# Optimization experiments

Hardware: AMD Instinct MI355X
Metric: run time of the kernel (lower is better)

## Reference

```python
import jax, jax.numpy as jnp
import numpy as np

D_MODEL = 1024
N_HEADS = 16
D_K = D_MODEL // N_HEADS


def setup_inputs() -> dict:
    key = jax.random.key(0)
    ks = jax.random.split(key, 11)
    B, S = 2, 2048
    scale = 1.0 / np.sqrt(D_MODEL)
    inp = {
        "q": jax.random.normal(ks[0], (B, S, D_MODEL), jnp.float32),
        "k": jax.random.normal(ks[1], (B, S, D_MODEL), jnp.float32),
        "v": jax.random.normal(ks[2], (B, S, D_MODEL), jnp.float32),
        "w_q": jax.random.normal(ks[3], (D_MODEL, D_MODEL), jnp.float32) * scale,
        "b_q": jnp.zeros((D_MODEL,), jnp.float32),
        "w_k": jax.random.normal(ks[4], (D_MODEL, D_MODEL), jnp.float32) * scale,
        "b_k": jnp.zeros((D_MODEL,), jnp.float32),
        "w_v": jax.random.normal(ks[5], (D_MODEL, D_MODEL), jnp.float32) * scale,
        "b_v": jnp.zeros((D_MODEL,), jnp.float32),
        "w_o": jax.random.normal(ks[6], (D_MODEL, D_MODEL), jnp.float32) * scale,
        "b_o": jnp.zeros((D_MODEL,), jnp.float32),
    }
    return inp


def reference(q, k, v, w_q, b_q, w_k, b_k, w_v, b_v, w_o, b_o):
    B, S, _ = q.shape
    # Linear projections (torch Linear: x @ W.T + b), split heads -> [B, H, S, d_k]
    def proj(x, w, b):
        y = x @ w.T + b
        return y.reshape(B, -1, N_HEADS, D_K).transpose(0, 2, 1, 3)

    qh = proj(q, w_q, b_q)
    kh = proj(k, w_k, b_k)
    vh = proj(v, w_v, b_v)

    scores = jnp.einsum("bhsd,bhtd->bhst", qh, kh) / np.sqrt(D_K)  # [B,H,S,S]
    attn = jax.nn.softmax(scores, axis=-1)  # dropout is identity at eval
    out = jnp.einsum("bhst,bhtd->bhsd", attn, vh)  # [B,H,S,d_k]
    out = out.transpose(0, 2, 1, 3).reshape(B, S, N_HEADS * D_K)
    return out @ w_o.T + b_o
```

## Files before the change

kernel.cpp:

```cpp
#include <hip/hip_runtime.h>
#include <cstdint>


typedef float  f32x4   __attribute__((ext_vector_type(4)));
typedef float  f32x16  __attribute__((ext_vector_type(16)));
typedef __bf16 bf16x8  __attribute__((ext_vector_type(8)));
typedef unsigned short u16;
typedef u16 u16x4 __attribute__((ext_vector_type(4)));
typedef u16 u16x8 __attribute__((ext_vector_type(8)));

#define D_MODEL 1024
#define SEQ     2048
#define BATCH   2
#define NH      16
#define DKH     64
#define MTOT    (BATCH * SEQ)
#define KVB     64
#define QBLK    256
#define HSTRIDE ((size_t)SEQ * DKH)

#if __has_builtin(__builtin_amdgcn_exp2f)
#define EXP2(x) __builtin_amdgcn_exp2f(x)
#else
#define EXP2(x) exp2f(x)
#endif

__device__ __forceinline__ u16 f2bf(float f) {
  uint32_t u = __builtin_bit_cast(uint32_t, f);
  u = u + 0x7fffu + ((u >> 16) & 1u);
  return (u16)(u >> 16);
}
__device__ __forceinline__ u16 f2bf_hw(float f) {
  return __builtin_bit_cast(u16, (__bf16)f);
}

__device__ __forceinline__ void gl_lds16(const void* g, void* l) {
  __builtin_amdgcn_global_load_lds(
      (__attribute__((address_space(1))) void*)(g),
      (__attribute__((address_space(3))) void*)(l), 16, 0, 0);
}

__device__ __forceinline__ void cvt_body(const float* __restrict__ in,
                                         u16* __restrict__ out, int i) {
  float4 v = reinterpret_cast<const float4*>(in)[i];
  uint32_t p0 = (uint32_t)f2bf(v.x) | ((uint32_t)f2bf(v.y) << 16);
  uint32_t p1 = (uint32_t)f2bf(v.z) | ((uint32_t)f2bf(v.w) << 16);
  reinterpret_cast<uint2*>(out)[i] = make_uint2(p0, p1);
}

__global__ __launch_bounds__(256) void cvt_qkv(
    const float* q, const float* k, const float* v,
    u16* qb, u16* kb, u16* vb) {
  int z = blockIdx.y;
  const float* in = (z == 0) ? q : (z == 1) ? k : v;
  u16* out = (z == 0) ? qb : (z == 1) ? kb : vb;
  cvt_body(in, out, blockIdx.x * 256 + threadIdx.x);
}

__global__ __launch_bounds__(256) void cvt_w(
    const float* w0, const float* w1, const float* w2, const float* w3,
    u16* o0, u16* o1, u16* o2, u16* o3) {
  int z = blockIdx.y;
  const float* in = (z == 0) ? w0 : (z == 1) ? w1 : (z == 2) ? w2 : w3;
  u16* out = (z == 0) ? o0 : (z == 1) ? o1 : (z == 2) ? o2 : o3;
  cvt_body(in, out, blockIdx.x * 256 + threadIdx.x);
}

template <bool BF16OUT, bool HEADA, bool HEADC>
__device__ __forceinline__ void gemm_bt_body(
    const u16* __restrict__ A, const u16* __restrict__ W,
    const float* __restrict__ bias, void* __restrict__ Cout,
    int N, int K, float scale, int bidx) {
  __shared__ u16 As[128][64];
  __shared__ u16 Bs[128][64];
  const int nbx = N / 128;
  const int bx = bidx % nbx, by = bidx / nbx;
  const int tid = threadIdx.x, wave = tid >> 6, lane = tid & 63;
  const int l15 = lane & 15, lg = lane >> 4;
  const int wr = wave >> 1, wc = wave & 1;
  f32x4 acc[4][4] = {};
  const int rA = by * 128 + (lane >> 3);
  const int rB = bx * 128 + (lane >> 3);
  const int ccol = (lane & 7) * 8;

  for (int kt = 0; kt < K; kt += 64) {
    for (int c = wave; c < 16; c += 4) {
      if (HEADA) {
        int m = rA + 8 * c;
        size_t a_off = (size_t)((m >> 11) * NH + (kt >> 6)) * HSTRIDE +
                       (size_t)(m & (SEQ - 1)) * 64 + ccol;
        gl_lds16(A + a_off, &As[8 * c][0]);
      } else {
        gl_lds16(A + (size_t)(rA + 8 * c) * K + kt + ccol, &As[8 * c][0]);
      }
      gl_lds16(W + (size_t)(rB + 8 * c) * K + kt + ccol, &Bs[8 * c][0]);
    }
    __syncthreads();
#pragma unroll
    for (int kc = 0; kc < 2; ++kc) {
      bf16x8 af[4], bw[4];
#pragma unroll
      for (int m = 0; m < 4; ++m)
        af[m] = *(const bf16x8*)&As[wr * 64 + m * 16 + l15][kc * 32 + 8 * lg];
#pragma unroll
      for (int n = 0; n < 4; ++n)
        bw[n] = *(const bf16x8*)&Bs[wc * 64 + n * 16 + l15][kc * 32 + 8 * lg];
#pragma unroll
      for (int m = 0; m < 4; ++m)
#pragma unroll
        for (int n = 0; n < 4; ++n)
          acc[m][n] = __builtin_amdgcn_mfma_f32_16x16x32_bf16(
              af[m], bw[n], acc[m][n], 0, 0, 0);
    }
    __syncthreads();
  }
#pragma unroll
  for (int n = 0; n < 4; ++n) {
    int col = bx * 128 + wc * 64 + n * 16 + l15;
    float bv = bias[col];
#pragma unroll
    for (int m = 0; m < 4; ++m) {
      int row0 = by * 128 + wr * 64 + m * 16 + 4 * lg;
#pragma unroll
      for (int j = 0; j < 4; ++j) {
        float v = (acc[m][n][j] + bv) * scale;
        int row = row0 + j;
        if (HEADC) {
          size_t off = (size_t)((row >> 11) * NH + (col >> 6)) * HSTRIDE +
                       (size_t)(row & (SEQ - 1)) * 64 + (col & 63);
          ((u16*)Cout)[off] = f2bf(v);
        } else if (BF16OUT) {
          ((u16*)Cout)[(size_t)row * N + col] = f2bf(v);
        } else {
          ((float*)Cout)[(size_t)row * N + col] = v;
        }
      }
    }
  }
}

#define SCALE_Q 0.18033688011112042f

__global__ __launch_bounds__(256) void proj_kernel(
    const u16* qb, const u16* kb, const u16* vb,
    const u16* wq, const u16* wk, const u16* wv,
    const float* b_q, const float* b_k, const float* b_v,
    u16* Qp, u16* Kp, u16* Vp) {
  int z = blockIdx.y;
  const u16* A = (z == 0) ? qb : (z == 1) ? kb : vb;
  const u16* W = (z == 0) ? wq : (z == 1) ? wk : wv;
  const float* bi = (z == 0) ? b_q : (z == 1) ? b_k : b_v;
  u16* O = (z == 0) ? Qp : (z == 1) ? Kp : Vp;
  float scale = (z == 0) ? SCALE_Q : 1.0f;
  gemm_bt_body<true, false, true>(A, W, bi, O, D_MODEL, D_MODEL, scale,
                                  blockIdx.x);
}

__global__ __launch_bounds__(256) void oproj_kernel(
    const u16* Op, const u16* wo, const float* b_o, float* out) {
  gemm_bt_body<false, true, false>(Op, wo, b_o, out, D_MODEL, D_MODEL, 1.0f,
                                   blockIdx.x);
}

__global__ __launch_bounds__(512, 2) void attn_kernel(
    const u16* __restrict__ Qh, const u16* __restrict__ Kh,
    const u16* __restrict__ Vh, u16* __restrict__ Oh) {
  __shared__ u16 QPl[QBLK * 64];
  __shared__ u16 Ks[2][KVB * 64];
  __shared__ u16 Vt[2][64 * KVB];
  const int bid = blockIdx.x;
  const int g = bid & 31, qt = bid >> 5;
  const size_t base = (size_t)g * HSTRIDE;
  const int tid = threadIdx.x, wave = tid >> 6, lane = tid & 63;
  const int l31 = lane & 31, hi = lane >> 5;
  const int q0 = qt * QBLK;
  const int srow = lane >> 3;
  const int scol = 8 * ((lane & 7) ^ srow);

  for (int c = wave; c < 32; c += 8)
    gl_lds16(Qh + base + (size_t)(q0 + 8 * c + srow) * 64 + scol,
             QPl + 8 * c * 64);
  gl_lds16(Kh + base + (size_t)(8 * wave + srow) * 64 + scol,
           Ks[0] + 8 * wave * 64);
  const int vp = tid >> 4, vq = tid & 15;
  u16x4 va, vb;
  {
    const u16* vsrc = Vh + base + (size_t)(2 * vp) * 64 + vq * 4;
    va = *(const u16x4*)vsrc;
    vb = *(const u16x4*)(vsrc + 64);
  }
  asm volatile("s_waitcnt vmcnt(0)" ::: "memory");
  __syncthreads();
#pragma unroll
  for (int j = 0; j < 4; ++j) {
    int dk = vq * 4 + j;
    uint32_t wv = (uint32_t)va[j] | ((uint32_t)vb[j] << 16);
    *(uint32_t*)&Vt[0][dk * 64 + (((vp >> 2) ^ (vq & 7)) << 3) + (vp & 3) * 2] =
        wv;
  }
  __syncthreads();

  bf16x8 qf[4];
#pragma unroll
  for (int kk = 0; kk < 4; ++kk) {
    int row = wave * 32 + l31;
    qf[kk] = *(const bf16x8*)&QPl[row * 64 + (((2 * kk + hi) ^ (row & 7)) << 3)];
  }
  u16* Pw = QPl + wave * 32 * 64;

  float mrow = -3e38f, lrow = 0.f;
  f32x16 acc[2] = {};

  for (int kt = 0; kt < SEQ / KVB; ++kt) {
    const int cur = kt & 1, nxt = cur ^ 1;
    if (kt + 1 < SEQ / KVB) {
      const size_t kv0 = base + (size_t)(kt + 1) * KVB * 64;
      gl_lds16(Kh + kv0 + (size_t)(8 * wave + srow) * 64 + scol,
               Ks[nxt] + 8 * wave * 64);
      const u16* vsrc = Vh + kv0 + (size_t)(2 * vp) * 64 + vq * 4;
      va = *(const u16x4*)vsrc;
      vb = *(const u16x4*)(vsrc + 64);
    }
    f32x16 s[2] = {};
#pragma unroll
    for (int t = 0; t < 2; ++t)
#pragma unroll
      for (int kk = 0; kk < 4; ++kk) {
        int row = t * 32 + l31;
        bf16x8 kf = *(const bf16x8*)&Ks[cur][row * 64 +
                                             (((2 * kk + hi) ^ (row & 7)) << 3)];
        s[t] = __builtin_amdgcn_mfma_f32_32x32x16_bf16(kf, qf[kk], s[t], 0, 0, 0);
      }
    float mx[16];
#pragma unroll
    for (int r = 0; r < 16; ++r) mx[r] = fmaxf(s[0][r], s[1][r]);
#pragma unroll
    for (int st2 = 8; st2 >= 1; st2 >>= 1)
#pragma unroll
      for (int r = 0; r < st2; ++r) mx[r] = fmaxf(mx[r], mx[r + st2]);
    float mtile = fmaxf(mx[0], __shfl_xor(mx[0], 32, 64));
    float mnew = fmaxf(mrow, mtile);
    float corr = EXP2(mrow - mnew);
    mrow = mnew;
    float sm0 = 0.f, sm1 = 0.f, sm2 = 0.f, sm3 = 0.f;
#pragma unroll
    for (int t = 0; t < 2; ++t)
#pragma unroll
      for (int r = 0; r < 16; r += 4) {
        float p0 = EXP2(s[t][r] - mnew);
        float p1 = EXP2(s[t][r + 1] - mnew);
        float p2 = EXP2(s[t][r + 2] - mnew);
        float p3 = EXP2(s[t][r + 3] - mnew);
        s[t][r] = p0; s[t][r + 1] = p1; s[t][r + 2] = p2; s[t][r + 3] = p3;
        sm0 += p0; sm1 += p1; sm2 += p2; sm3 += p3;
      }
    float psum = (sm0 + sm1) + (sm2 + sm3);
    lrow = lrow * corr + (psum + __shfl_xor(psum, 32, 64));
#pragma unroll
    for (int nd = 0; nd < 2; ++nd)
#pragma unroll
      for (int r = 0; r < 16; ++r) acc[nd][r] *= corr;

#pragma unroll
    for (int t = 0; t < 2; ++t)
#pragma unroll
      for (int b2 = 0; b2 < 4; ++b2) {
        u16x4 pk = {f2bf_hw(s[t][4 * b2]), f2bf_hw(s[t][4 * b2 + 1]),
                    f2bf_hw(s[t][4 * b2 + 2]), f2bf_hw(s[t][4 * b2 + 3])};
        *(u16x4*)&Pw[l31 * 64 + (((4 * t + b2) ^ (l31 & 7)) << 3) + 4 * hi] = pk;
      }
#pragma unroll
    for (int ks = 0; ks < 4; ++ks) {
      bf16x8 pf =
          *(const bf16x8*)&Pw[l31 * 64 + (((2 * ks + hi) ^ (l31 & 7)) << 3)];
#pragma unroll
      for (int nd = 0; nd < 2; ++nd) {
        int dkr = nd * 32 + l31;
        bf16x8 vf = *(const bf16x8*)&Vt[cur][dkr * 64 +
                        (((2 * ks + hi) ^ ((l31 >> 2) & 7)) << 3)];
        acc[nd] =
            __builtin_amdgcn_mfma_f32_32x32x16_bf16(vf, pf, acc[nd], 0, 0, 0);
      }
    }
    asm volatile("s_waitcnt vmcnt(0)" ::: "memory");
    __syncthreads();
    if (kt + 1 < SEQ / KVB) {
#pragma unroll
      for (int j = 0; j < 4; ++j) {
        int dk = vq * 4 + j;
        uint32_t wv = (uint32_t)va[j] | ((uint32_t)vb[j] << 16);
        *(uint32_t*)&Vt[nxt][dk * 64 + (((vp >> 2) ^ (vq & 7)) << 3) +
                             (vp & 3) * 2] = wv;
      }
    }
    __syncthreads();
  }

  float rinv = 1.0f / lrow;
  u16* Os = QPl;
  {
    int row = wave * 32 + l31;
#pragma unroll
    for (int nd = 0; nd < 2; ++nd)
#pragma unroll
      for (int b2 = 0; b2 < 4; ++b2) {
        u16x4 ok = {f2bf_hw(acc[nd][4 * b2] * rinv),
                    f2bf_hw(acc[nd][4 * b2 + 1] * rinv),
                    f2bf_hw(acc[nd][4 * b2 + 2] * rinv),
                    f2bf_hw(acc[nd][4 * b2 + 3] * rinv)};
        *(u16x4*)&Os[row * 64 + (((4 * nd + b2) ^ (row & 7)) << 3) + 4 * hi] =
            ok;
      }
  }
  __syncthreads();
  {
    const int row = tid >> 1, half = tid & 1;
    u16* gp = (u16*)(Oh + base + (size_t)(q0 + row) * 64 + half * 32);
#pragma unroll
    for (int c2 = 0; c2 < 4; ++c2) {
      int pc = (half * 4 + c2) ^ (row & 7);
      *(u16x8*)(gp + c2 * 8) = *(const u16x8*)&Os[row * 64 + pc * 8];
    }
  }
}

extern "C" void kernel_launch(void* const* d_in, const int* in_sizes, int n_in,
                              void* d_out, int out_size, void* d_ws,
                              size_t ws_size, hipStream_t stream) {
  (void)in_sizes; (void)n_in; (void)out_size; (void)ws_size;
  const float* q   = (const float*)d_in[0];
  const float* k   = (const float*)d_in[1];
  const float* v   = (const float*)d_in[2];
  const float* w_q = (const float*)d_in[3];
  const float* b_q = (const float*)d_in[4];
  const float* w_k = (const float*)d_in[5];
  const float* b_k = (const float*)d_in[6];
  const float* w_v = (const float*)d_in[7];
  const float* b_v = (const float*)d_in[8];
  const float* w_o = (const float*)d_in[9];
  const float* b_o = (const float*)d_in[10];
  float* out = (float*)d_out;

  const size_t ACT = (size_t)MTOT * D_MODEL;
  const size_t WEL = (size_t)D_MODEL * D_MODEL;
  u16* qb  = (u16*)d_ws;
  u16* kb  = qb + ACT;
  u16* vb  = kb + ACT;
  u16* wqb = vb + ACT;
  u16* wkb = wqb + WEL;
  u16* wvb = wkb + WEL;
  u16* wob = wvb + WEL;
  u16* Qp  = wob + WEL;
  u16* Kp  = Qp + ACT;
  u16* Vp  = Kp + ACT;
  u16* Op  = Vp + ACT;

  const int na = (int)(ACT / 4), nw = (int)(WEL / 4);
  cvt_qkv<<<dim3(na / 256, 3), 256, 0, stream>>>(q, k, v, qb, kb, vb);
  cvt_w<<<dim3(nw / 256, 4), 256, 0, stream>>>(w_q, w_k, w_v, w_o,
                                               wqb, wkb, wvb, wob);

  proj_kernel<<<dim3((MTOT / 128) * (D_MODEL / 128), 3), 256, 0, stream>>>(
      qb, kb, vb, wqb, wkb, wvb, b_q, b_k, b_v, Qp, Kp, Vp);

  attn_kernel<<<dim3(BATCH * NH * (SEQ / QBLK)), 512, 0, stream>>>(Qp, Kp, Vp,
                                                                   Op);

  oproj_kernel<<<dim3((MTOT / 128) * (D_MODEL / 128)), 256, 0, stream>>>(
      Op, wob, b_o, out);
}
```

Before: 249.0 us.

## Split KV range across wave halves, lazy rescale, merge conversion kernels

The attention kernel now uses a 128-row Q block. Its 8 waves split into two halves that each cover half of the KV sequence, and their partial softmax states are merged through LDS at the end. This doubles the grid and raises occupancy (launch bounds 4). It also adds lazy max rescaling that skips the correction unless the tile max grows by more than 8, sets MFMA priority hints, and replaces the async K prefetch with register-staged loads. The two fp32-to-bf16 conversion launches are merged into one. The costs are an extra merge step and more sync per tile, and the lazy rescale lets exponentials reach up to 2^8, which is a precision risk.

Result: slower. 293.0 us (+17.7%).

```diff
diff --git a/kernel.cpp b/kernel.cpp
--- a/kernel.cpp
+++ b/kernel.cpp
@@ -16,7 +16,7 @@
 #define DKH     64
 #define MTOT    (BATCH * SEQ)
 #define KVB     64
-#define QBLK    256
+#define QBLK    128
 #define HSTRIDE ((size_t)SEQ * DKH)
 
 #if __has_builtin(__builtin_amdgcn_exp2f)
@@ -48,22 +48,23 @@
   reinterpret_cast<uint2*>(out)[i] = make_uint2(p0, p1);
 }
 
-__global__ __launch_bounds__(256) void cvt_qkv(
+__global__ __launch_bounds__(256) void cvt_all(
     const float* q, const float* k, const float* v,
-    u16* qb, u16* kb, u16* vb) {
-  int z = blockIdx.y;
-  const float* in = (z == 0) ? q : (z == 1) ? k : v;
-  u16* out = (z == 0) ? qb : (z == 1) ? kb : vb;
-  cvt_body(in, out, blockIdx.x * 256 + threadIdx.x);
-}
-
-__global__ __launch_bounds__(256) void cvt_w(
     const float* w0, const float* w1, const float* w2, const float* w3,
-    u16* o0, u16* o1, u16* o2, u16* o3) {
-  int z = blockIdx.y;
-  const float* in = (z == 0) ? w0 : (z == 1) ? w1 : (z == 2) ? w2 : w3;
-  u16* out = (z == 0) ? o0 : (z == 1) ? o1 : (z == 2) ? o2 : o3;
-  cvt_body(in, out, blockIdx.x * 256 + threadIdx.x);
+    u16* qb, u16* kb, u16* vb, u16* o0, u16* o1, u16* o2, u16* o3) {
+  const int NA = 1 << 20, NW = 1 << 18;
+  int i = blockIdx.x * 256 + threadIdx.x;
+  const float* src; u16* dst; int r;
+  if (i < 3 * NA) {
+    int s = i >> 20; r = i & (NA - 1);
+    src = (s == 0) ? q : (s == 1) ? k : v;
+    dst = (s == 0) ? qb : (s == 1) ? kb : vb;
+  } else {
+    int j = i - 3 * NA; int s = j >> 18; r = j & (NW - 1);
+    src = (s == 0) ? w0 : (s == 1) ? w1 : (s == 2) ? w2 : w3;
+    dst = (s == 0) ? o0 : (s == 1) ? o1 : (s == 2) ? o2 : o3;
+  }
+  cvt_body(src, dst, r);
 }
 
 template <bool BF16OUT, bool HEADA, bool HEADC>
@@ -162,75 +163,90 @@
                                    blockIdx.x);
 }
 
-__global__ __launch_bounds__(512, 2) void attn_kernel(
+__global__ __launch_bounds__(512, 4) void attn_kernel(
     const u16* __restrict__ Qh, const u16* __restrict__ Kh,
     const u16* __restrict__ Vh, u16* __restrict__ Oh) {
-  __shared__ u16 QPl[QBLK * 64];
-  __shared__ u16 Ks[2][KVB * 64];
-  __shared__ u16 Vt[2][64 * KVB];
+  __shared__ u16 QPl[16384];
+  __shared__ u16 Ks[2][4096];
+  __shared__ u16 Vt[2][4096];
   const int bid = blockIdx.x;
   const int g = bid & 31, qt = bid >> 5;
   const size_t base = (size_t)g * HSTRIDE;
   const int tid = threadIdx.x, wave = tid >> 6, lane = tid & 63;
   const int l31 = lane & 31, hi = lane >> 5;
+  const int qg = wave & 3, half = wave >> 2;
   const int q0 = qt * QBLK;
   const int srow = lane >> 3;
   const int scol = 8 * ((lane & 7) ^ srow);
 
-  for (int c = wave; c < 32; c += 8)
+  const int ht = tid & 255;
+  const int kr = ht >> 2, kc4 = ht & 3;
+  const int vp2 = ht >> 3, vd8 = (ht & 7) * 8;
+  const size_t kvbase = base + (size_t)(half * (SEQ / 2)) * 64;
+
+  for (int c = wave; c < 16; c += 8)
     gl_lds16(Qh + base + (size_t)(q0 + 8 * c + srow) * 64 + scol,
              QPl + 8 * c * 64);
-  gl_lds16(Kh + base + (size_t)(8 * wave + srow) * 64 + scol,
-           Ks[0] + 8 * wave * 64);
-  const int vp = tid >> 4, vq = tid & 15;
-  u16x4 va, vb;
+  u16x8 kra, krb, va, vb;
   {
-    const u16* vsrc = Vh + base + (size_t)(2 * vp) * 64 + vq * 4;
-    va = *(const u16x4*)vsrc;
-    vb = *(const u16x4*)(vsrc + 64);
+    const u16* ks = Kh + kvbase + (size_t)kr * 64 + kc4 * 16;
+    kra = *(const u16x8*)ks;
+    krb = *(const u16x8*)(ks + 8);
+    const u16* vs = Vh + kvbase + (size_t)(2 * vp2) * 64 + vd8;
+    va = *(const u16x8*)vs;
+    vb = *(const u16x8*)(vs + 64);
   }
   asm volatile("s_waitcnt vmcnt(0)" ::: "memory");
   __syncthreads();
-#pragma unroll
-  for (int j = 0; j < 4; ++j) {
-    int dk = vq * 4 + j;
-    uint32_t wv = (uint32_t)va[j] | ((uint32_t)vb[j] << 16);
-    *(uint32_t*)&Vt[0][dk * 64 + (((vp >> 2) ^ (vq & 7)) << 3) + (vp & 3) * 2] =
-        wv;
-  }
+#define STORE_KV()                                                         \
+  {                                                                        \
+    *(u16x8*)&Ks[half][kr * 64 + (((2 * kc4) ^ (kr & 7)) << 3)] = kra;     \
+    *(u16x8*)&Ks[half][kr * 64 + (((2 * kc4 + 1) ^ (kr & 7)) << 3)] = krb; \
+    _Pragma("unroll") for (int d = 0; d < 8; ++d) {                        \
+      int dk = vd8 + d;                                                    \
+      uint32_t wv = (uint32_t)va[d] | ((uint32_t)vb[d] << 16);             \
+      *(uint32_t*)&Vt[half][dk * 64 + (((vp2 >> 2) ^ ((dk >> 2) & 7)) << 3) + \
+                            (vp2 & 3) * 2] = wv;                           \
+    }                                                                      \
+  }
+  STORE_KV();
   __syncthreads();
 
   bf16x8 qf[4];
 #pragma unroll
   for (int kk = 0; kk < 4; ++kk) {
-    int row = wave * 32 + l31;
+    int row = qg * 32 + l31;
     qf[kk] = *(const bf16x8*)&QPl[row * 64 + (((2 * kk + hi) ^ (row & 7)) << 3)];
   }
-  u16* Pw = QPl + wave * 32 * 64;
+  __syncthreads();
+  u16* Pw = QPl + wave * 2048;
 
   float mrow = -3e38f, lrow = 0.f;
   f32x16 acc[2] = {};
-
-  for (int kt = 0; kt < SEQ / KVB; ++kt) {
-    const int cur = kt & 1, nxt = cur ^ 1;
-    if (kt + 1 < SEQ / KVB) {
-      const size_t kv0 = base + (size_t)(kt + 1) * KVB * 64;
-      gl_lds16(Kh + kv0 + (size_t)(8 * wave + srow) * 64 + scol,
-               Ks[nxt] + 8 * wave * 64);
-      const u16* vsrc = Vh + kv0 + (size_t)(2 * vp) * 64 + vq * 4;
-      va = *(const u16x4*)vsrc;
-      vb = *(const u16x4*)(vsrc + 64);
+  const int NT = (SEQ / 2) / KVB;
+
+  for (int kt = 0; kt < NT; ++kt) {
+    if (kt + 1 < NT) {
+      const size_t kvo = kvbase + (size_t)(kt + 1) * KVB * 64;
+      const u16* ks = Kh + kvo + (size_t)kr * 64 + kc4 * 16;
+      kra = *(const u16x8*)ks;
+      krb = *(const u16x8*)(ks + 8);
+      const u16* vs = Vh + kvo + (size_t)(2 * vp2) * 64 + vd8;
+      va = *(const u16x8*)vs;
+      vb = *(const u16x8*)(vs + 64);
     }
     f32x16 s[2] = {};
+    __builtin_amdgcn_s_setprio(1);
 #pragma unroll
     for (int t = 0; t < 2; ++t)
 #pragma unroll
       for (int kk = 0; kk < 4; ++kk) {
         int row = t * 32 + l31;
-        bf16x8 kf = *(const bf16x8*)&Ks[cur][row * 64 +
-                                             (((2 * kk + hi) ^ (row & 7)) << 3)];
+        bf16x8 kf = *(const bf16x8*)&Ks[half][row * 64 +
+                                              (((2 * kk + hi) ^ (row & 7)) << 3)];
         s[t] = __builtin_amdgcn_mfma_f32_32x32x16_bf16(kf, qf[kk], s[t], 0, 0, 0);
       }
+    __builtin_amdgcn_s_setprio(0);
     float mx[16];
 #pragma unroll
     for (int r = 0; r < 16; ++r) mx[r] = fmaxf(s[0][r], s[1][r]);
@@ -239,27 +255,29 @@
 #pragma unroll
       for (int r = 0; r < st2; ++r) mx[r] = fmaxf(mx[r], mx[r + st2]);
     float mtile = fmaxf(mx[0], __shfl_xor(mx[0], 32, 64));
-    float mnew = fmaxf(mrow, mtile);
-    float corr = EXP2(mrow - mnew);
-    mrow = mnew;
+    if (mtile > mrow + 8.0f) {
+      float corr = EXP2(mrow - mtile);
+      mrow = mtile;
+      lrow *= corr;
+#pragma unroll
+      for (int nd = 0; nd < 2; ++nd)
+#pragma unroll
+        for (int r = 0; r < 16; ++r) acc[nd][r] *= corr;
+    }
     float sm0 = 0.f, sm1 = 0.f, sm2 = 0.f, sm3 = 0.f;
 #pragma unroll
     for (int t = 0; t < 2; ++t)
 #pragma unroll
       for (int r = 0; r < 16; r += 4) {
-        float p0 = EXP2(s[t][r] - mnew);
-        float p1 = EXP2(s[t][r + 1] - mnew);
-        float p2 = EXP2(s[t][r + 2] - mnew);
-        float p3 = EXP2(s[t][r + 3] - mnew);
+        float p0 = EXP2(s[t][r] - mrow);
+        float p1 = EXP2(s[t][r + 1] - mrow);
+        float p2 = EXP2(s[t][r + 2] - mrow);
+        float p3 = EXP2(s[t][r + 3] - mrow);
         s[t][r] = p0; s[t][r + 1] = p1; s[t][r + 2] = p2; s[t][r + 3] = p3;
         sm0 += p0; sm1 += p1; sm2 += p2; sm3 += p3;
       }
     float psum = (sm0 + sm1) + (sm2 + sm3);
-    lrow = lrow * corr + (psum + __shfl_xor(psum, 32, 64));
-#pragma unroll
-    for (int nd = 0; nd < 2; ++nd)
-#pragma unroll
-      for (int r = 0; r < 16; ++r) acc[nd][r] *= corr;
+    lrow += psum + __shfl_xor(psum, 32, 64);
 
 #pragma unroll
     for (int t = 0; t < 2; ++t)
@@ -269,36 +287,57 @@
                     f2bf_hw(s[t][4 * b2 + 2]), f2bf_hw(s[t][4 * b2 + 3])};
         *(u16x4*)&Pw[l31 * 64 + (((4 * t + b2) ^ (l31 & 7)) << 3) + 4 * hi] = pk;
       }
-#pragma unroll
-    for (int ks = 0; ks < 4; ++ks) {
+    __builtin_amdgcn_s_setprio(1);
+#pragma unroll
+    for (int ks2 = 0; ks2 < 4; ++ks2) {
       bf16x8 pf =
-          *(const bf16x8*)&Pw[l31 * 64 + (((2 * ks + hi) ^ (l31 & 7)) << 3)];
+          *(const bf16x8*)&Pw[l31 * 64 + (((2 * ks2 + hi) ^ (l31 & 7)) << 3)];
 #pragma unroll
       for (int nd = 0; nd < 2; ++nd) {
         int dkr = nd * 32 + l31;
-        bf16x8 vf = *(const bf16x8*)&Vt[cur][dkr * 64 +
-                        (((2 * ks + hi) ^ ((l31 >> 2) & 7)) << 3)];
+        bf16x8 vf = *(const bf16x8*)&Vt[half][dkr * 64 +
+                        (((2 * ks2 + hi) ^ ((l31 >> 2) & 7)) << 3)];
         acc[nd] =
             __builtin_amdgcn_mfma_f32_32x32x16_bf16(vf, pf, acc[nd], 0, 0, 0);
       }
     }
-    asm volatile("s_waitcnt vmcnt(0)" ::: "memory");
+    __builtin_amdgcn_s_setprio(0);
     __syncthreads();
-    if (kt + 1 < SEQ / KVB) {
-#pragma unroll
-      for (int j = 0; j < 4; ++j) {
-        int dk = vq * 4 + j;
-        uint32_t wv = (uint32_t)va[j] | ((uint32_t)vb[j] << 16);
-        *(uint32_t*)&Vt[nxt][dk * 64 + (((vp >> 2) ^ (vq & 7)) << 3) +
-                             (vp & 3) * 2] = wv;
-      }
-    }
+    if (kt + 1 < NT) STORE_KV();
     __syncthreads();
   }
 
-  float rinv = 1.0f / lrow;
-  u16* Os = QPl;
-  {
+  float* MA = (float*)QPl;
+  float* ML = (float*)Vt;
+  if (wave >= 4) {
+    int u = wave - 4;
+#pragma unroll
+    for (int j = 0; j < 8; ++j) {
+      f32x4 qd = {acc[j >> 2][4 * (j & 3)], acc[j >> 2][4 * (j & 3) + 1],
+                  acc[j >> 2][4 * (j & 3) + 2], acc[j >> 2][4 * (j & 3) + 3]};
+      *(f32x4*)&MA[u * 2048 + lane * 32 + ((j ^ (lane & 7)) << 2)] = qd;
+    }
+    ML[u * 128 + lane * 2] = mrow;
+    ML[u * 128 + lane * 2 + 1] = lrow;
+  }
+  __syncthreads();
+  u16* Os = &Ks[0][0];
+  if (wave < 4) {
+    float mb = ML[wave * 128 + lane * 2];
+    float lb = ML[wave * 128 + lane * 2 + 1];
+    float m2 = fmaxf(mrow, mb);
+    float ca = EXP2(mrow - m2), cb = EXP2(mb - m2);
+    lrow = lrow * ca + lb * cb;
+#pragma unroll
+    for (int j = 0; j < 8; ++j) {
+      f32x4 qd = *(const f32x4*)&MA[wave * 2048 + lane * 32 +
+                                    ((j ^ (lane & 7)) << 2)];
+#pragma unroll
+      for (int m = 0; m < 4; ++m)
+        acc[j >> 2][4 * (j & 3) + m] =
+            acc[j >> 2][4 * (j & 3) + m] * ca + qd[m] * cb;
+    }
+    float rinv = 1.0f / lrow;
     int row = wave * 32 + l31;
 #pragma unroll
     for (int nd = 0; nd < 2; ++nd)
@@ -314,12 +353,13 @@
   }
   __syncthreads();
   {
-    const int row = tid >> 1, half = tid & 1;
-    u16* gp = (u16*)(Oh + base + (size_t)(q0 + row) * 64 + half * 32);
-#pragma unroll
-    for (int c2 = 0; c2 < 4; ++c2) {
-      int pc = (half * 4 + c2) ^ (row & 7);
-      *(u16x8*)(gp + c2 * 8) = *(const u16x8*)&Os[row * 64 + pc * 8];
+    const int row = tid >> 2, cq = tid & 3;
+    u16* gp = (u16*)(Oh + base + (size_t)(q0 + row) * 64);
+#pragma unroll
+    for (int e = 0; e < 2; ++e) {
+      int c = 2 * cq + e;
+      *(u16x8*)(gp + c * 8) =
+          *(const u16x8*)&Os[row * 64 + ((c ^ (row & 7)) << 3)];
     }
   }
 }
@@ -355,10 +395,9 @@
   u16* Vp  = Kp + ACT;
   u16* Op  = Vp + ACT;
 
-  const int na = (int)(ACT / 4), nw = (int)(WEL / 4);
-  cvt_qkv<<<dim3(na / 256, 3), 256, 0, stream>>>(q, k, v, qb, kb, vb);
-  cvt_w<<<dim3(nw / 256, 4), 256, 0, stream>>>(w_q, w_k, w_v, w_o,
-                                               wqb, wkb, wvb, wob);
+  const int nq = (int)((3 * ACT + 4 * WEL) / 4);
+  cvt_all<<<nq / 256, 256, 0, stream>>>(q, k, v, w_q, w_k, w_v, w_o,
+                                        qb, kb, vb, wqb, wkb, wvb, wob);
 
   proj_kernel<<<dim3((MTOT / 128) * (D_MODEL / 128), 3), 256, 0, stream>>>(
       qb, kb, vb, wqb, wkb, wvb, b_q, b_k, b_v, Qp, Kp, Vp);
```

## Double KV tile per iteration, lazy softmax rescale, setprio, merged convert kernel

Applied to the files above, without the earlier changes.

The attention loop now handles 128 keys per iteration as two 64-key sub-tiles, which halves the number of barriers and loop iterations, with K/V LDS buffers grown to match. The online-softmax rescale of the accumulator and row sum is skipped unless some row's max has grown by more than 8 in log2 units. MFMA sections are wrapped in s_setprio to favour matrix issue. The two fp32-to-bf16 conversion kernels are merged into one launch. The costs are more LDS per block, which may reduce occupancy at 2 blocks per CU, and a softmax whose exponentials can reach up to 2^8 before rescaling.

New measurement: 243.9 us. -2.1%, faster.

```diff
diff --git a/kernel.cpp b/kernel.cpp
--- a/kernel.cpp
+++ b/kernel.cpp
@@ -15,7 +15,6 @@
 #define NH      16
 #define DKH     64
 #define MTOT    (BATCH * SEQ)
-#define KVB     64
 #define QBLK    256
 #define HSTRIDE ((size_t)SEQ * DKH)
 
@@ -48,22 +47,23 @@
   reinterpret_cast<uint2*>(out)[i] = make_uint2(p0, p1);
 }
 
-__global__ __launch_bounds__(256) void cvt_qkv(
+__global__ __launch_bounds__(256) void cvt_all(
     const float* q, const float* k, const float* v,
-    u16* qb, u16* kb, u16* vb) {
-  int z = blockIdx.y;
-  const float* in = (z == 0) ? q : (z == 1) ? k : v;
-  u16* out = (z == 0) ? qb : (z == 1) ? kb : vb;
-  cvt_body(in, out, blockIdx.x * 256 + threadIdx.x);
-}
-
-__global__ __launch_bounds__(256) void cvt_w(
     const float* w0, const float* w1, const float* w2, const float* w3,
-    u16* o0, u16* o1, u16* o2, u16* o3) {
-  int z = blockIdx.y;
-  const float* in = (z == 0) ? w0 : (z == 1) ? w1 : (z == 2) ? w2 : w3;
-  u16* out = (z == 0) ? o0 : (z == 1) ? o1 : (z == 2) ? o2 : o3;
-  cvt_body(in, out, blockIdx.x * 256 + threadIdx.x);
+    u16* qb, u16* kb, u16* vb, u16* o0, u16* o1, u16* o2, u16* o3) {
+  const int NA = 1 << 20, NW = 1 << 18;
+  int i = blockIdx.x * 256 + threadIdx.x;
+  const float* src; u16* dst; int r;
+  if (i < 3 * NA) {
+    int s = i >> 20; r = i & (NA - 1);
+    src = (s == 0) ? q : (s == 1) ? k : v;
+    dst = (s == 0) ? qb : (s == 1) ? kb : vb;
+  } else {
+    int j = i - 3 * NA; int s = j >> 18; r = j & (NW - 1);
+    src = (s == 0) ? w0 : (s == 1) ? w1 : (s == 2) ? w2 : w3;
+    dst = (s == 0) ? o0 : (s == 1) ? o1 : (s == 2) ? o2 : o3;
+  }
+  cvt_body(src, dst, r);
 }
 
 template <bool BF16OUT, bool HEADA, bool HEADC>
@@ -166,8 +166,8 @@
     const u16* __restrict__ Qh, const u16* __restrict__ Kh,
     const u16* __restrict__ Vh, u16* __restrict__ Oh) {
   __shared__ u16 QPl[QBLK * 64];
-  __shared__ u16 Ks[2][KVB * 64];
-  __shared__ u16 Vt[2][64 * KVB];
+  __shared__ u16 Ks[2][2][64 * 64];
+  __shared__ u16 Vt[2][2][64 * 64];
   const int bid = blockIdx.x;
   const int g = bid & 31, qt = bid >> 5;
   const size_t base = (size_t)g * HSTRIDE;
@@ -181,23 +181,31 @@
     gl_lds16(Qh + base + (size_t)(q0 + 8 * c + srow) * 64 + scol,
              QPl + 8 * c * 64);
   gl_lds16(Kh + base + (size_t)(8 * wave + srow) * 64 + scol,
-           Ks[0] + 8 * wave * 64);
+           &Ks[0][0][8 * wave * 64]);
+  gl_lds16(Kh + base + 4096 + (size_t)(8 * wave + srow) * 64 + scol,
+           &Ks[0][1][8 * wave * 64]);
   const int vp = tid >> 4, vq = tid & 15;
-  u16x4 va, vb;
+  u16x4 va, vb, vc, vd;
   {
-    const u16* vsrc = Vh + base + (size_t)(2 * vp) * 64 + vq * 4;
-    va = *(const u16x4*)vsrc;
-    vb = *(const u16x4*)(vsrc + 64);
+    const u16* vs = Vh + base + (size_t)(2 * vp) * 64 + vq * 4;
+    va = *(const u16x4*)vs;
+    vb = *(const u16x4*)(vs + 64);
+    vc = *(const u16x4*)(vs + 4096);
+    vd = *(const u16x4*)(vs + 4096 + 64);
   }
   asm volatile("s_waitcnt vmcnt(0)" ::: "memory");
   __syncthreads();
-#pragma unroll
-  for (int j = 0; j < 4; ++j) {
-    int dk = vq * 4 + j;
-    uint32_t wv = (uint32_t)va[j] | ((uint32_t)vb[j] << 16);
-    *(uint32_t*)&Vt[0][dk * 64 + (((vp >> 2) ^ (vq & 7)) << 3) + (vp & 3) * 2] =
-        wv;
-  }
+#define STORE_V(BUF, SUB, RA, RB)                                             \
+  {                                                                           \
+    _Pragma("unroll") for (int j = 0; j < 4; ++j) {                           \
+      int dk = vq * 4 + j;                                                    \
+      uint32_t wv = (uint32_t)RA[j] | ((uint32_t)RB[j] << 16);                \
+      *(uint32_t*)&Vt[BUF][SUB][dk * 64 + (((vp >> 2) ^ (vq & 7)) << 3) +     \
+                               (vp & 3) * 2] = wv;                            \
+    }                                                                         \
+  }
+  STORE_V(0, 0, va, vb);
+  STORE_V(0, 1, vc, vd);
   __syncthreads();
 
   bf16x8 qf[4];
@@ -210,88 +218,105 @@
 
   float mrow = -3e38f, lrow = 0.f;
   f32x16 acc[2] = {};
-
-  for (int kt = 0; kt < SEQ / KVB; ++kt) {
+  const int NT = SEQ / 128;
+
+  for (int kt = 0; kt < NT; ++kt) {
     const int cur = kt & 1, nxt = cur ^ 1;
-    if (kt + 1 < SEQ / KVB) {
-      const size_t kv0 = base + (size_t)(kt + 1) * KVB * 64;
+    if (kt + 1 < NT) {
+      const size_t kv0 = base + (size_t)(kt + 1) * 128 * 64;
       gl_lds16(Kh + kv0 + (size_t)(8 * wave + srow) * 64 + scol,
-               Ks[nxt] + 8 * wave * 64);
-      const u16* vsrc = Vh + kv0 + (size_t)(2 * vp) * 64 + vq * 4;
-      va = *(const u16x4*)vsrc;
-      vb = *(const u16x4*)(vsrc + 64);
-    }
-    f32x16 s[2] = {};
+               &Ks[nxt][0][8 * wave * 64]);
+      gl_lds16(Kh + kv0 + 4096 + (size_t)(8 * wave + srow) * 64 + scol,
+               &Ks[nxt][1][8 * wave * 64]);
+      const u16* vs = Vh + kv0 + (size_t)(2 * vp) * 64 + vq * 4;
+      va = *(const u16x4*)vs;
+      vb = *(const u16x4*)(vs + 64);
+      vc = *(const u16x4*)(vs + 4096);
+      vd = *(const u16x4*)(vs + 4096 + 64);
+    }
+    f32x16 s0[2] = {}, s1[2] = {};
+    __builtin_amdgcn_s_setprio(1);
 #pragma unroll
     for (int t = 0; t < 2; ++t)
 #pragma unroll
       for (int kk = 0; kk < 4; ++kk) {
         int row = t * 32 + l31;
-        bf16x8 kf = *(const bf16x8*)&Ks[cur][row * 64 +
-                                             (((2 * kk + hi) ^ (row & 7)) << 3)];
-        s[t] = __builtin_amdgcn_mfma_f32_32x32x16_bf16(kf, qf[kk], s[t], 0, 0, 0);
-      }
+        int off = row * 64 + (((2 * kk + hi) ^ (row & 7)) << 3);
+        s0[t] = __builtin_amdgcn_mfma_f32_32x32x16_bf16(
+            *(const bf16x8*)&Ks[cur][0][off], qf[kk], s0[t], 0, 0, 0);
+        s1[t] = __builtin_amdgcn_mfma_f32_32x32x16_bf16(
+            *(const bf16x8*)&Ks[cur][1][off], qf[kk], s1[t], 0, 0, 0);
+      }
+    __builtin_amdgcn_s_setprio(0);
     float mx[16];
 #pragma unroll
-    for (int r = 0; r < 16; ++r) mx[r] = fmaxf(s[0][r], s[1][r]);
+    for (int r = 0; r < 16; ++r)
+      mx[r] = fmaxf(fmaxf(s0[0][r], s0[1][r]), fmaxf(s1[0][r], s1[1][r]));
 #pragma unroll
     for (int st2 = 8; st2 >= 1; st2 >>= 1)
 #pragma unroll
       for (int r = 0; r < st2; ++r) mx[r] = fmaxf(mx[r], mx[r + st2]);
     float mtile = fmaxf(mx[0], __shfl_xor(mx[0], 32, 64));
-    float mnew = fmaxf(mrow, mtile);
-    float corr = EXP2(mrow - mnew);
-    mrow = mnew;
-    float sm0 = 0.f, sm1 = 0.f, sm2 = 0.f, sm3 = 0.f;
+    if (!__all(mtile - mrow <= 8.0f)) {
+      float mnew = fmaxf(mrow, mtile);
+      float corr = EXP2(mrow - mnew);
+      mrow = mnew;
+      lrow *= corr;
+#pragma unroll
+      for (int nd = 0; nd < 2; ++nd)
+#pragma unroll
+        for (int r = 0; r < 16; ++r) acc[nd][r] *= corr;
+    }
+    float sma = 0.f, smb = 0.f, smc = 0.f, smd = 0.f;
 #pragma unroll
     for (int t = 0; t < 2; ++t)
 #pragma unroll
       for (int r = 0; r < 16; r += 4) {
-        float p0 = EXP2(s[t][r] - mnew);
-        float p1 = EXP2(s[t][r + 1] - mnew);
-        float p2 = EXP2(s[t][r + 2] - mnew);
-        float p3 = EXP2(s[t][r + 3] - mnew);
-        s[t][r] = p0; s[t][r + 1] = p1; s[t][r + 2] = p2; s[t][r + 3] = p3;
-        sm0 += p0; sm1 += p1; sm2 += p2; sm3 += p3;
-      }
-    float psum = (sm0 + sm1) + (sm2 + sm3);
-    lrow = lrow * corr + (psum + __shfl_xor(psum, 32, 64));
-#pragma unroll
-    for (int nd = 0; nd < 2; ++nd)
-#pragma unroll
-      for (int r = 0; r < 16; ++r) acc[nd][r] *= corr;
-
-#pragma unroll
-    for (int t = 0; t < 2; ++t)
-#pragma unroll
-      for (int b2 = 0; b2 < 4; ++b2) {
-        u16x4 pk = {f2bf_hw(s[t][4 * b2]), f2bf_hw(s[t][4 * b2 + 1]),
-                    f2bf_hw(s[t][4 * b2 + 2]), f2bf_hw(s[t][4 * b2 + 3])};
-        *(u16x4*)&Pw[l31 * 64 + (((4 * t + b2) ^ (l31 & 7)) << 3) + 4 * hi] = pk;
-      }
-#pragma unroll
-    for (int ks = 0; ks < 4; ++ks) {
-      bf16x8 pf =
-          *(const bf16x8*)&Pw[l31 * 64 + (((2 * ks + hi) ^ (l31 & 7)) << 3)];
-#pragma unroll
-      for (int nd = 0; nd < 2; ++nd) {
-        int dkr = nd * 32 + l31;
-        bf16x8 vf = *(const bf16x8*)&Vt[cur][dkr * 64 +
-                        (((2 * ks + hi) ^ ((l31 >> 2) & 7)) << 3)];
-        acc[nd] =
-            __builtin_amdgcn_mfma_f32_32x32x16_bf16(vf, pf, acc[nd], 0, 0, 0);
-      }
+        float a0 = EXP2(s0[t][r] - mrow), a1 = EXP2(s0[t][r + 1] - mrow);
+        float a2 = EXP2(s0[t][r + 2] - mrow), a3 = EXP2(s0[t][r + 3] - mrow);
+        s0[t][r] = a0; s0[t][r + 1] = a1; s0[t][r + 2] = a2; s0[t][r + 3] = a3;
+        sma += a0; smb += a1; smc += a2; smd += a3;
+        float b0 = EXP2(s1[t][r] - mrow), b1 = EXP2(s1[t][r + 1] - mrow);
+        float b2 = EXP2(s1[t][r + 2] - mrow), b3 = EXP2(s1[t][r + 3] - mrow);
+        s1[t][r] = b0; s1[t][r + 1] = b1; s1[t][r + 2] = b2; s1[t][r + 3] = b3;
+        sma += b0; smb += b1; smc += b2; smd += b3;
+      }
+    float psum = (sma + smb) + (smc + smd);
+    lrow += psum + __shfl_xor(psum, 32, 64);
+
+#pragma unroll
+    for (int sub = 0; sub < 2; ++sub) {
+      f32x16* sp = (sub == 0) ? s0 : s1;
+#pragma unroll
+      for (int t = 0; t < 2; ++t)
+#pragma unroll
+        for (int b2 = 0; b2 < 4; ++b2) {
+          u16x4 pk = {f2bf_hw(sp[t][4 * b2]), f2bf_hw(sp[t][4 * b2 + 1]),
+                      f2bf_hw(sp[t][4 * b2 + 2]), f2bf_hw(sp[t][4 * b2 + 3])};
+          *(u16x4*)&Pw[l31 * 64 + (((4 * t + b2) ^ (l31 & 7)) << 3) + 4 * hi] =
+              pk;
+        }
+      __builtin_amdgcn_s_setprio(1);
+#pragma unroll
+      for (int ks2 = 0; ks2 < 4; ++ks2) {
+        bf16x8 pf =
+            *(const bf16x8*)&Pw[l31 * 64 + (((2 * ks2 + hi) ^ (l31 & 7)) << 3)];
+#pragma unroll
+        for (int nd = 0; nd < 2; ++nd) {
+          int dkr = nd * 32 + l31;
+          bf16x8 vf = *(const bf16x8*)&Vt[cur][sub][dkr * 64 +
+                          (((2 * ks2 + hi) ^ ((l31 >> 2) & 7)) << 3)];
+          acc[nd] =
+              __builtin_amdgcn_mfma_f32_32x32x16_bf16(vf, pf, acc[nd], 0, 0, 0);
+        }
+      }
+      __builtin_amdgcn_s_setprio(0);
     }
     asm volatile("s_waitcnt vmcnt(0)" ::: "memory");
     __syncthreads();
-    if (kt + 1 < SEQ / KVB) {
-#pragma unroll
-      for (int j = 0; j < 4; ++j) {
-        int dk = vq * 4 + j;
-        uint32_t wv = (uint32_t)va[j] | ((uint32_t)vb[j] << 16);
-        *(uint32_t*)&Vt[nxt][dk * 64 + (((vp >> 2) ^ (vq & 7)) << 3) +
-                             (vp & 3) * 2] = wv;
-      }
+    if (kt + 1 < NT) {
+      STORE_V(nxt, 0, va, vb);
+      STORE_V(nxt, 1, vc, vd);
     }
     __syncthreads();
   }
@@ -355,10 +380,9 @@
   u16* Vp  = Kp + ACT;
   u16* Op  = Vp + ACT;
 
-  const int na = (int)(ACT / 4), nw = (int)(WEL / 4);
-  cvt_qkv<<<dim3(na / 256, 3), 256, 0, stream>>>(q, k, v, qb, kb, vb);
-  cvt_w<<<dim3(nw / 256, 4), 256, 0, stream>>>(w_q, w_k, w_v, w_o,
-                                               wqb, wkb, wvb, wob);
+  const int nq = (int)((3 * ACT + 4 * WEL) / 4);
+  cvt_all<<<nq / 256, 256, 0, stream>>>(q, k, v, w_q, w_k, w_v, w_o,
+                                        qb, kb, vb, wqb, wkb, wvb, wob);
 
   proj_kernel<<<dim3((MTOT / 128) * (D_MODEL / 128), 3), 256, 0, stream>>>(
       qb, kb, vb, wqb, wkb, wvb, b_q, b_k, b_v, Qp, Kp, Vp);
```
